# Kernel tuning notes

Hardware: AMD Instinct MI355X
Metric: run time of the kernel (lower is better)

## Reference

```python
import jax, jax.numpy as jnp
import numpy as np

N_NODES = 50000
N_EDGES = 800000
D_IN = 128
DIM = 128
N_LAYERS = 3
N_GRAPHS = 128


def setup_inputs() -> dict:
    key = jax.random.key(0)
    ks = jax.random.split(key, 10)
    x = jax.random.normal(ks[0], (N_NODES, D_IN), dtype=jnp.float32)
    edge_index = jax.random.randint(ks[1], (2, N_EDGES), 0, N_NODES, dtype=jnp.int64)
    batch = jnp.sort(jax.random.randint(ks[2], (N_NODES,), 0, N_GRAPHS, dtype=jnp.int64))
    def glorot(k, fan_in, fan_out):
        s = jnp.sqrt(6.0 / (fan_in + fan_out))
        return jax.random.uniform(k, (fan_in, fan_out), jnp.float32, -s, s)
    W0 = glorot(ks[3], D_IN, DIM)
    W1 = glorot(ks[4], DIM, DIM)
    W2 = glorot(ks[5], DIM, DIM)
    b0 = jnp.zeros((DIM,), jnp.float32)
    b1 = jnp.zeros((DIM,), jnp.float32)
    b2 = jnp.zeros((DIM,), jnp.float32)
    return {"x": x, "edge_index": edge_index, "batch": batch,
            "W0": W0, "b0": b0, "W1": W1, "b1": b1, "W2": W2, "b2": b2}


def _gcn_norm(edge_index, n_nodes):
    # add self-loops, then symmetric normalization (PyG gcn_norm)
    loops = jnp.arange(n_nodes, dtype=edge_index.dtype)
    src = jnp.concatenate([edge_index[0], loops])
    dst = jnp.concatenate([edge_index[1], loops])
    deg = jax.ops.segment_sum(jnp.ones_like(dst, dtype=jnp.float32), dst,
                              num_segments=n_nodes)
    dinv = jnp.where(deg > 0, jax.lax.rsqrt(deg), 0.0)
    norm = dinv[src] * dinv[dst]  # [E + N]
    return src, dst, norm


def _gcn_conv(x, W, b, src, dst, norm, n_nodes):
    h = x @ W                      # [N, dim]
    msgs = h[src] * norm[:, None]  # [E+N, dim] gather + edge scale
    out = jax.ops.segment_sum(msgs, dst, num_segments=n_nodes)  # scatter-add
    return out + b


def reference(x, edge_index, batch, W0, b0, W1, b1, W2, b2):
    n = x.shape[0]
    src, dst, norm = _gcn_norm(edge_index, n)
    Ws, bs = (W0, W1, W2), (b0, b1, b2)
    xs = []
    h = x
    for i in range(N_LAYERS):
        h = jax.nn.relu(_gcn_conv(h, Ws[i], bs[i], src, dst, norm, n))
        xs.append(h)
    # global mean pool per layer output
    counts = jax.ops.segment_sum(jnp.ones((n,), jnp.float32), batch,
                                 num_segments=N_GRAPHS)
    counts = jnp.maximum(counts, 1.0)[:, None]
    xpool = [jax.ops.segment_sum(h, batch, num_segments=N_GRAPHS) / counts
             for h in xs]
    return jnp.concatenate(xpool, axis=1), jnp.concatenate(xs, axis=1)
```

## Files before the change

kernel.cpp:

```cpp
#include <hip/hip_runtime.h>

#define NNODES 50000
#define NEDGES 800000
#define DIM 128
#define NGRAPHS 128
#define OUT1_STRIDE 384
#define OUT0_ELEMS (NGRAPHS * OUT1_STRIDE)
#define SCAN_CHUNK 512
#define ROWPAD 50048

typedef unsigned int uint;
typedef unsigned short ushort;
typedef short bf16x8 __attribute__((ext_vector_type(8)));
typedef float f32x4 __attribute__((ext_vector_type(4)));

union U4 { uint4 u; bf16x8 h; };

__device__ inline uint rne_bf16(float f) {
    uint b = __float_as_uint(f);
    return (b + 0x7fffu + ((b >> 16) & 1u)) >> 16;
}
__device__ inline uint pack_bf16(float lo, float hi) {
    return rne_bf16(lo) | (rne_bf16(hi) << 16);
}
__device__ inline float blo(uint u) { return __uint_as_float(u << 16); }
__device__ inline float bhi(uint u) { return __uint_as_float(u & 0xffff0000u); }

__global__ __launch_bounds__(256) void k_pre(const float* __restrict__ W0,
                                             const float* __restrict__ W1,
                                             const float* __restrict__ W2,
                                             uint* __restrict__ wz,
                                             int* __restrict__ rowcnt, int N) {
    if (blockIdx.x >= 24) {
        int i = (blockIdx.x - 24) * 256 + threadIdx.x;
        if (i < N) rowcnt[i] = 0;
        return;
    }
    int layer = blockIdx.x >> 3;
    const float* W = (layer == 0) ? W0 : ((layer == 1) ? W1 : W2);
    int t = (blockIdx.x & 7) * 256 + threadIdx.x;
    int f = t >> 6, lane = t & 63;
    int kb = f >> 3, nt = f & 7;
    int q = lane >> 4, m = lane & 15;
    int col = nt * 16 + m;
    uint v[8];
#pragma unroll
    for (int j = 0; j < 8; ++j)
        v[j] = rne_bf16(W[(kb * 32 + q * 8 + j) * 128 + col]);
    uint4 o;
    o.x = v[0] | (v[1] << 16);
    o.y = v[2] | (v[3] << 16);
    o.z = v[4] | (v[5] << 16);
    o.w = v[6] | (v[7] << 16);
    ((uint4*)wz)[layer * 2048 + t] = o;
}

__global__ void k_count(const int* __restrict__ dst, int* __restrict__ rowcnt,
                        int* __restrict__ rank, int E) {
    int e = blockIdx.x * blockDim.x + threadIdx.x;
    if (e < E) rank[e] = atomicAdd(&rowcnt[dst[e]], 1);
}

__global__ __launch_bounds__(512) void k_sum(const int* __restrict__ cnt,
                                             int* __restrict__ bsum,
                                             float* __restrict__ dinv, int n) {
    __shared__ int red[512];
    int t = threadIdx.x;
    int i = blockIdx.x * SCAN_CHUNK + t;
    int c = (i < n) ? cnt[i] : 0;
    if (i < n) dinv[i] = rsqrtf((float)c + 1.0f);
    red[t] = c;
    __syncthreads();
    for (int off = 256; off > 0; off >>= 1) {
        if (t < off) red[t] += red[t + off];
        __syncthreads();
    }
    if (t == 0) bsum[blockIdx.x] = red[0];
}

__global__ __launch_bounds__(128) void k_scanb(const int* __restrict__ bsum,
                                               int* __restrict__ boff, int nb) {
    __shared__ int s[128];
    int t = threadIdx.x;
    int v = (t < nb) ? bsum[t] : 0;
    s[t] = v;
    __syncthreads();
    for (int off = 1; off < 128; off <<= 1) {
        int u = (t >= off) ? s[t - off] : 0;
        __syncthreads();
        s[t] += u;
        __syncthreads();
    }
    boff[t] = s[t] - v;
    if (t == nb - 1) boff[nb] = s[t];
}

__global__ __launch_bounds__(512) void k_writeptr(const int* __restrict__ cnt,
                                                  const int* __restrict__ boff,
                                                  int* __restrict__ rowptr, int n) {
    __shared__ int s[512];
    int t = threadIdx.x;
    int i = blockIdx.x * SCAN_CHUNK + t;
    int v = (i < n) ? cnt[i] : 0;
    s[t] = v;
    __syncthreads();
    for (int off = 1; off < 512; off <<= 1) {
        int u = (t >= off) ? s[t - off] : 0;
        __syncthreads();
        s[t] += u;
        __syncthreads();
    }
    if (i < n) rowptr[i] = boff[blockIdx.x] + s[t] - v;
    if (i == n - 1) rowptr[n] = boff[blockIdx.x] + s[t];
}

__global__ void k_fill(const int* __restrict__ src, const int* __restrict__ dst,
                       const int* __restrict__ rowptr, const int* __restrict__ rank,
                       int* __restrict__ csr_src, int E) {
    int e = blockIdx.x * blockDim.x + threadIdx.x;
    if (e < E) {
        int d = dst[e];
        csr_src[rowptr[d] + rank[e]] = src[e];
    }
}

__global__ __launch_bounds__(256) void k_gemm(const float* __restrict__ A, int lda,
                                              const uint* __restrict__ Wswz,
                                              const float* __restrict__ dinv,
                                              uint* __restrict__ hb, int M) {
    __shared__ uint4 wsw[2048];
    __shared__ ushort cbuf[64 * 128];
    int tid = threadIdx.x;
#pragma unroll
    for (int i = 0; i < 8; ++i)
        wsw[i * 256 + tid] = ((const uint4*)Wswz)[i * 256 + tid];
    __syncthreads();
    int wave = tid >> 6, lane = tid & 63;
    int q = lane >> 4, m = lane & 15;
    int row0 = blockIdx.x * 64 + wave * 16;
    int arow = min(row0 + m, M - 1);
    const float* Ar = A + (size_t)arow * lda + q * 8;
    f32x4 zero = {0.0f, 0.0f, 0.0f, 0.0f};
    f32x4 acc[8];
#pragma unroll
    for (int i = 0; i < 8; ++i) acc[i] = zero;
#pragma unroll
    for (int kb = 0; kb < 4; ++kb) {
        float4 f0 = *(const float4*)(Ar + kb * 32);
        float4 f1 = *(const float4*)(Ar + kb * 32 + 4);
        U4 a;
        a.u.x = pack_bf16(f0.x, f0.y);
        a.u.y = pack_bf16(f0.z, f0.w);
        a.u.z = pack_bf16(f1.x, f1.y);
        a.u.w = pack_bf16(f1.z, f1.w);
#pragma unroll
        for (int nt = 0; nt < 8; ++nt) {
            U4 b; b.u = wsw[(kb * 8 + nt) * 64 + lane];
            acc[nt] = __builtin_amdgcn_mfma_f32_16x16x32_bf16(a.h, b.h, acc[nt], 0, 0, 0);
        }
    }
    float dv[4];
#pragma unroll
    for (int r = 0; r < 4; ++r)
        dv[r] = dinv[min(row0 + q * 4 + r, M - 1)];
    ushort* cw = cbuf + wave * 16 * 128;
#pragma unroll
    for (int nt = 0; nt < 8; ++nt)
#pragma unroll
        for (int r = 0; r < 4; ++r)
            cw[(q * 4 + r) * 128 + nt * 16 + m] = (ushort)rne_bf16(acc[nt][r] * dv[r]);
    __syncthreads();
    const uint4* cr4 = (const uint4*)cbuf;
#pragma unroll
    for (int i = 0; i < 4; ++i) {
        int c = (wave * 256) + i * 64 + lane;
        int grow = blockIdx.x * 64 + (c >> 4);
        uint4 v = cr4[c];
        if (grow < M) ((uint4*)hb)[(size_t)grow * 16 + (c & 15)] = v;
    }
}

__global__ __launch_bounds__(256) void k_agg(const uint* __restrict__ hb,
                                             const int* __restrict__ rowptr,
                                             const int* __restrict__ csr_src,
                                             const float* __restrict__ dinv,
                                             const float* __restrict__ bias,
                                             float* __restrict__ out1,
                                             int N, int layer) {
    int wave = threadIdx.x >> 6;
    int lane = threadIdx.x & 63;
    int n = blockIdx.x * 4 + wave;
    if (n >= N) return;
    float din = dinv[n];
    uint u = hb[(size_t)n * 64 + lane];
    float ax = blo(u);
    float ay = bhi(u);
    int beg = rowptr[n], end = rowptr[n + 1];
    for (int base = beg; base < end; base += 64) {
        int cnt = min(64, end - base);
        int eidx = base + lane;
        int smy = (eidx < end) ? csr_src[eidx] : 0;
        int j = 0;
        for (; j + 8 <= cnt; j += 8) {
            int s0 = __shfl(smy, j),     s1 = __shfl(smy, j + 1);
            int s2 = __shfl(smy, j + 2), s3 = __shfl(smy, j + 3);
            int s4 = __shfl(smy, j + 4), s5 = __shfl(smy, j + 5);
            int s6 = __shfl(smy, j + 6), s7 = __shfl(smy, j + 7);
            uint u0 = hb[(size_t)s0 * 64 + lane];
            uint u1 = hb[(size_t)s1 * 64 + lane];
            uint u2 = hb[(size_t)s2 * 64 + lane];
            uint u3 = hb[(size_t)s3 * 64 + lane];
            uint u4 = hb[(size_t)s4 * 64 + lane];
            uint u5 = hb[(size_t)s5 * 64 + lane];
            uint u6 = hb[(size_t)s6 * 64 + lane];
            uint u7 = hb[(size_t)s7 * 64 + lane];
            ax += ((blo(u0) + blo(u1)) + (blo(u2) + blo(u3)))
                + ((blo(u4) + blo(u5)) + (blo(u6) + blo(u7)));
            ay += ((bhi(u0) + bhi(u1)) + (bhi(u2) + bhi(u3)))
                + ((bhi(u4) + bhi(u5)) + (bhi(u6) + bhi(u7)));
        }
        for (; j + 4 <= cnt; j += 4) {
            int s0 = __shfl(smy, j),     s1 = __shfl(smy, j + 1);
            int s2 = __shfl(smy, j + 2), s3 = __shfl(smy, j + 3);
            uint u0 = hb[(size_t)s0 * 64 + lane];
            uint u1 = hb[(size_t)s1 * 64 + lane];
            uint u2 = hb[(size_t)s2 * 64 + lane];
            uint u3 = hb[(size_t)s3 * 64 + lane];
            ax += (blo(u0) + blo(u1)) + (blo(u2) + blo(u3));
            ay += (bhi(u0) + bhi(u1)) + (bhi(u2) + bhi(u3));
        }
        for (; j < cnt; ++j) {
            int ss = __shfl(smy, j);
            uint uu = hb[(size_t)ss * 64 + lane];
            ax += blo(uu);
            ay += bhi(uu);
        }
    }
    float2 b = ((const float2*)bias)[lane];
    float ox = fmaxf(din * ax + b.x, 0.0f);
    float oy = fmaxf(din * ay + b.y, 0.0f);
    size_t o1 = (size_t)n * OUT1_STRIDE + layer * DIM + lane * 2;
    *(float2*)(out1 + o1) = make_float2(ox, oy);
}

__global__ __launch_bounds__(256) void k_pool(const float* __restrict__ out1,
                                              const int* __restrict__ batch,
                                              float* __restrict__ out0, int N) {
    int g = blockIdx.x / 3;
    int chunk = blockIdx.x % 3;
    int lo = 0, hi = N;
    while (lo < hi) { int mid = (lo + hi) >> 1; if (batch[mid] < g) lo = mid + 1; else hi = mid; }
    int beg = lo;
    hi = N;
    while (lo < hi) { int mid = (lo + hi) >> 1; if (batch[mid] < g + 1) lo = mid + 1; else hi = mid; }
    int end = lo;
    int t = threadIdx.x;
    int ch = t & 127;
    int slice = t >> 7;
    const float* p = out1 + (size_t)chunk * 128 + ch;
    float acc = 0.0f;
    int i = beg + slice;
    for (; i + 6 < end; i += 8) {
        float a0 = p[(size_t)i * OUT1_STRIDE];
        float a1 = p[(size_t)(i + 2) * OUT1_STRIDE];
        float a2 = p[(size_t)(i + 4) * OUT1_STRIDE];
        float a3 = p[(size_t)(i + 6) * OUT1_STRIDE];
        acc += (a0 + a1) + (a2 + a3);
    }
    for (; i < end; i += 2) acc += p[(size_t)i * OUT1_STRIDE];
    __shared__ float red[256];
    red[t] = acc;
    __syncthreads();
    if (t < 128) {
        float tot = red[t] + red[t + 128];
        float cnt = (float)(end - beg);
        out0[(size_t)g * OUT1_STRIDE + chunk * 128 + t] = tot / fmaxf(cnt, 1.0f);
    }
}

extern "C" void kernel_launch(void* const* d_in, const int* in_sizes, int n_in,
                              void* d_out, int out_size, void* d_ws, size_t ws_size,
                              hipStream_t stream) {
    const float* x     = (const float*)d_in[0];
    const int*   ei    = (const int*)d_in[1];
    const int*   batch = (const int*)d_in[2];
    const float* W0 = (const float*)d_in[3];
    const float* b0 = (const float*)d_in[4];
    const float* W1 = (const float*)d_in[5];
    const float* b1 = (const float*)d_in[6];
    const float* W2 = (const float*)d_in[7];
    const float* b2 = (const float*)d_in[8];
    (void)n_in; (void)ws_size; (void)out_size;

    const int E = in_sizes[1] / 2;
    const int N = in_sizes[2];
    const int* src = ei;
    const int* dst = ei + E;

    char* ws = (char*)d_ws;
    uint*  hb       = (uint*)ws;  ws += (size_t)ROWPAD * 64 * 4;
    uint*  wz       = (uint*)ws;  ws += 3 * 8192 * 4;
    float* dinv     = (float*)ws; ws += 50016 * 4;
    int*   rowcnt   = (int*)ws;   ws += 50016 * 4;
    int*   rowptr   = (int*)ws;   ws += 50016 * 4;
    int*   rank     = (int*)ws;   ws += (size_t)NEDGES * 4;
    int*   csr_src  = (int*)ws;   ws += (size_t)NEDGES * 4;
    int*   bsum     = (int*)ws;   ws += 256 * 4;
    int*   boff     = (int*)ws;   ws += 256 * 4;

    float* out0 = (float*)d_out;
    float* out1 = (float*)d_out + OUT0_ELEMS;

    const int nb  = (N + SCAN_CHUNK - 1) / SCAN_CHUNK;
    const int nbz = 24 + (N + 255) / 256;

    k_pre     <<<nbz, 256, 0, stream>>>(W0, W1, W2, wz, rowcnt, N);
    k_count   <<<(E + 255) / 256, 256, 0, stream>>>(dst, rowcnt, rank, E);
    k_sum     <<<nb, 512, 0, stream>>>(rowcnt, bsum, dinv, N);
    k_scanb   <<<1, 128, 0, stream>>>(bsum, boff, nb);
    k_writeptr<<<nb, 512, 0, stream>>>(rowcnt, boff, rowptr, N);
    k_fill    <<<(E + 255) / 256, 256, 0, stream>>>(src, dst, rowptr, rank, csr_src, E);

    const float* bs[3] = {b0, b1, b2};
    const int ngb = (N + 63) / 64;
    for (int l = 0; l < 3; ++l) {
        const float* Ain = (l == 0) ? x : (out1 + (size_t)(l - 1) * DIM);
        int lda          = (l == 0) ? DIM : OUT1_STRIDE;
        k_gemm<<<ngb, 256, 0, stream>>>(Ain, lda, wz + l * 8192, dinv, hb, N);
        k_agg <<<(N + 3) / 4, 256, 0, stream>>>(hb, rowptr, csr_src, dinv,
                                                bs[l], out1, N, l);
    }
    k_pool<<<NGRAPHS * 3, 256, 0, stream>>>(out1, batch, out0, N);
}
```

Baseline: 314.1 us.

## Gather 16-byte row chunks in aggregation with 4 edges per wave step

The aggregation kernel is restructured so each wave splits into four 16-lane groups. Each group loads one neighbor's full 256-byte bf16 row with uint4 loads, so four edges are gathered per iteration, and the groups' partial sums are then reduced with xor shuffles. A zeroed padding row at index N is added and used as the target for out-of-range edges, which removes the tail loops. This is meant to use wider loads and have more gathers in flight per wave, at the cost of a cross-group reduction and wasted padding loads on nodes with low degree.

```diff
diff --git a/kernel.cpp b/kernel.cpp
--- a/kernel.cpp
+++ b/kernel.cpp
@@ -30,10 +30,12 @@
                                              const float* __restrict__ W1,
                                              const float* __restrict__ W2,
                                              uint* __restrict__ wz,
-                                             int* __restrict__ rowcnt, int N) {
+                                             int* __restrict__ rowcnt,
+                                             uint* __restrict__ hb, int N) {
     if (blockIdx.x >= 24) {
         int i = (blockIdx.x - 24) * 256 + threadIdx.x;
         if (i < N) rowcnt[i] = 0;
+        if (i < 64) hb[(size_t)N * 64 + i] = 0;
         return;
     }
     int layer = blockIdx.x >> 3;
@@ -191,55 +193,59 @@
     int lane = threadIdx.x & 63;
     int n = blockIdx.x * 4 + wave;
     if (n >= N) return;
+    int g16 = lane >> 4;
+    int m16 = lane & 15;
+    const uint4* hb4 = (const uint4*)hb;
+
+    uint4 su = hb4[(size_t)n * 16 + m16];
+    float sel = (g16 == 0) ? 1.0f : 0.0f;
+    float a0 = sel * blo(su.x), a1 = sel * bhi(su.x);
+    float a2 = sel * blo(su.y), a3 = sel * bhi(su.y);
+    float a4 = sel * blo(su.z), a5 = sel * bhi(su.z);
+    float a6 = sel * blo(su.w), a7 = sel * bhi(su.w);
+
+    int beg = rowptr[n], end = rowptr[n + 1];
+    for (int base = beg; base < end; base += 16) {
+        int s0, s1, s2, s3;
+        {
+            int e0 = base + 0 + g16;
+            int e1 = base + 4 + g16;
+            int e2 = base + 8 + g16;
+            int e3 = base + 12 + g16;
+            s0 = (e0 < end) ? csr_src[e0] : N;
+            s1 = (e1 < end) ? csr_src[min(e1, end - 1)] : N;
+            s2 = (e2 < end) ? csr_src[min(e2, end - 1)] : N;
+            s3 = (e3 < end) ? csr_src[min(e3, end - 1)] : N;
+        }
+        uint4 u0 = hb4[(size_t)s0 * 16 + m16];
+        uint4 u1 = hb4[(size_t)s1 * 16 + m16];
+        uint4 u2 = hb4[(size_t)s2 * 16 + m16];
+        uint4 u3 = hb4[(size_t)s3 * 16 + m16];
+        a0 += blo(u0.x); a1 += bhi(u0.x); a2 += blo(u0.y); a3 += bhi(u0.y);
+        a4 += blo(u0.z); a5 += bhi(u0.z); a6 += blo(u0.w); a7 += bhi(u0.w);
+        a0 += blo(u1.x); a1 += bhi(u1.x); a2 += blo(u1.y); a3 += bhi(u1.y);
+        a4 += blo(u1.z); a5 += bhi(u1.z); a6 += blo(u1.w); a7 += bhi(u1.w);
+        a0 += blo(u2.x); a1 += bhi(u2.x); a2 += blo(u2.y); a3 += bhi(u2.y);
+        a4 += blo(u2.z); a5 += bhi(u2.z); a6 += blo(u2.w); a7 += bhi(u2.w);
+        a0 += blo(u3.x); a1 += bhi(u3.x); a2 += blo(u3.y); a3 += bhi(u3.y);
+        a4 += blo(u3.z); a5 += bhi(u3.z); a6 += blo(u3.w); a7 += bhi(u3.w);
+    }
+
+#pragma unroll
+    for (int d = 16; d < 64; d <<= 1) {
+        a0 += __shfl_xor(a0, d); a1 += __shfl_xor(a1, d);
+        a2 += __shfl_xor(a2, d); a3 += __shfl_xor(a3, d);
+        a4 += __shfl_xor(a4, d); a5 += __shfl_xor(a5, d);
+        a6 += __shfl_xor(a6, d); a7 += __shfl_xor(a7, d);
+    }
+
+    float vx = (g16 == 0) ? a0 : (g16 == 1) ? a2 : (g16 == 2) ? a4 : a6;
+    float vy = (g16 == 0) ? a1 : (g16 == 1) ? a3 : (g16 == 2) ? a5 : a7;
     float din = dinv[n];
-    uint u = hb[(size_t)n * 64 + lane];
-    float ax = blo(u);
-    float ay = bhi(u);
-    int beg = rowptr[n], end = rowptr[n + 1];
-    for (int base = beg; base < end; base += 64) {
-        int cnt = min(64, end - base);
-        int eidx = base + lane;
-        int smy = (eidx < end) ? csr_src[eidx] : 0;
-        int j = 0;
-        for (; j + 8 <= cnt; j += 8) {
-            int s0 = __shfl(smy, j),     s1 = __shfl(smy, j + 1);
-            int s2 = __shfl(smy, j + 2), s3 = __shfl(smy, j + 3);
-            int s4 = __shfl(smy, j + 4), s5 = __shfl(smy, j + 5);
-            int s6 = __shfl(smy, j + 6), s7 = __shfl(smy, j + 7);
-            uint u0 = hb[(size_t)s0 * 64 + lane];
-            uint u1 = hb[(size_t)s1 * 64 + lane];
-            uint u2 = hb[(size_t)s2 * 64 + lane];
-            uint u3 = hb[(size_t)s3 * 64 + lane];
-            uint u4 = hb[(size_t)s4 * 64 + lane];
-            uint u5 = hb[(size_t)s5 * 64 + lane];
-            uint u6 = hb[(size_t)s6 * 64 + lane];
-            uint u7 = hb[(size_t)s7 * 64 + lane];
-            ax += ((blo(u0) + blo(u1)) + (blo(u2) + blo(u3)))
-                + ((blo(u4) + blo(u5)) + (blo(u6) + blo(u7)));
-            ay += ((bhi(u0) + bhi(u1)) + (bhi(u2) + bhi(u3)))
-                + ((bhi(u4) + bhi(u5)) + (bhi(u6) + bhi(u7)));
-        }
-        for (; j + 4 <= cnt; j += 4) {
-            int s0 = __shfl(smy, j),     s1 = __shfl(smy, j + 1);
-            int s2 = __shfl(smy, j + 2), s3 = __shfl(smy, j + 3);
-            uint u0 = hb[(size_t)s0 * 64 + lane];
-            uint u1 = hb[(size_t)s1 * 64 + lane];
-            uint u2 = hb[(size_t)s2 * 64 + lane];
-            uint u3 = hb[(size_t)s3 * 64 + lane];
-            ax += (blo(u0) + blo(u1)) + (blo(u2) + blo(u3));
-            ay += (bhi(u0) + bhi(u1)) + (bhi(u2) + bhi(u3));
-        }
-        for (; j < cnt; ++j) {
-            int ss = __shfl(smy, j);
-            uint uu = hb[(size_t)ss * 64 + lane];
-            ax += blo(uu);
-            ay += bhi(uu);
-        }
-    }
-    float2 b = ((const float2*)bias)[lane];
-    float ox = fmaxf(din * ax + b.x, 0.0f);
-    float oy = fmaxf(din * ay + b.y, 0.0f);
-    size_t o1 = (size_t)n * OUT1_STRIDE + layer * DIM + lane * 2;
+    float2 b = ((const float2*)bias)[m16 * 4 + g16];
+    float ox = fmaxf(din * vx + b.x, 0.0f);
+    float oy = fmaxf(din * vy + b.y, 0.0f);
+    size_t o1 = (size_t)n * OUT1_STRIDE + layer * DIM + (m16 * 8 + g16 * 2);
     *(float2*)(out1 + o1) = make_float2(ox, oy);
 }
 
@@ -314,7 +320,7 @@
     const int nb  = (N + SCAN_CHUNK - 1) / SCAN_CHUNK;
     const int nbz = 24 + (N + 255) / 256;
 
-    k_pre     <<<nbz, 256, 0, stream>>>(W0, W1, W2, wz, rowcnt, N);
+    k_pre     <<<nbz, 256, 0, stream>>>(W0, W1, W2, wz, rowcnt, hb, N);
     k_count   <<<(E + 255) / 256, 256, 0, stream>>>(dst, rowcnt, rank, E);
     k_sum     <<<nb, 512, 0, stream>>>(rowcnt, bsum, dinv, N);
     k_scanb   <<<1, 128, 0, stream>>>(bsum, boff, nb);
```

After: 310.1 us. No clear change (-1.3%).
